# Performance work log

Measured on AMD Instinct MI355X. Metric: run time of the kernel, lower is better.

The kernel has to match this reference:

```python
import jax, jax.numpy as jnp
import numpy as np

REF_POSE = np.array([[213.33335876464844, 124.50563049316406], [190.504638671875, 115.11840057373047], [169.9791717529297, 101.77180480957031], [146.72341918945312, 96.25749206542969], [128.86770629882812, 87.2344970703125], [150.34292602539062, 101.61070251464844], [119.29926300048828, 98.73982238769531], [100.03463745117188, 99.74459838867188], [82.62400817871094, 101.2509536743164], [148.91049194335938, 112.71517181396484], [114.37303161621094, 113.20121002197266], [91.90096282958984, 116.49812316894531], [74.75020599365234, 119.37875366210938], [149.59658813476562, 124.09295654296875], [119.72419738769531, 126.36898040771484], [99.59107208251953, 129.40196228027344], [82.82524108886719, 131.584228515625], [154.55911254882812, 135.07681274414062], [133.8833770751953, 140.85983276367188], [120.45906066894531, 145.40306091308594], [106.21541595458984, 150.072265625]], dtype=np.float32)

SCALES = (0.25, 0.5, 1.0)
ORIENTATIONS = (0, 90, 180, 270)
INPUT_SIZE = (256, 256)          # (H, W)
ANCHOR_STRIDE = (1, 1)           # (y_stride, x_stride)
POS_TH = 0.5
KPT_SIGMA = 0.05                 # per-keypoint OKS falloff


def _generate_anchor_poses():
    # scale + rotate ref pose about its centroid -> [A, 21, 2]
    c = REF_POSE.mean(axis=0, keepdims=True)
    out = []
    for s in SCALES:
        for o in ORIENTATIONS:
            th = np.deg2rad(o)
            R = np.array([[np.cos(th), -np.sin(th)], [np.sin(th), np.cos(th)]], dtype=np.float32)
            out.append(c + s * (REF_POSE - c) @ R.T)
    return np.stack(out).astype(np.float32)


def _all_anchors(feat_h, feat_w):
    base = _generate_anchor_poses()                      # [A,21,2]
    w_ratio = INPUT_SIZE[1] / feat_w
    h_ratio = INPUT_SIZE[0] / feat_h
    sx = np.arange(0, feat_w, ANCHOR_STRIDE[1]) * w_ratio
    sy = np.arange(0, feat_h, ANCHOR_STRIDE[0]) * h_ratio
    gx, gy = np.meshgrid(sx, sy)
    shifts = np.stack([gx.ravel(), gy.ravel()], axis=1).astype(np.float32)  # [K,2]
    all_a = base[None, :, :, :] + shifts[:, None, None, :]                  # [K,A,21,2]
    return jnp.asarray(all_a.reshape(-1, 21, 2))                            # [K*A,21,2]


def _pose_oks(anchors, gt):
    # anchors [N,21,2], gt [B,2,21,3] -> OKS sim [B,N,2]
    d2 = jnp.sum((anchors[None, :, None, :, :] - gt[:, None, :, :, :2]) ** 2, axis=-1)  # [B,N,2,21]
    vis = (gt[..., 2] > 0).astype(anchors.dtype)[:, None, :, :]                          # [B,1,2,21]
    xy = gt[..., :2]
    area = jnp.prod(xy.max(axis=2) - xy.min(axis=2), axis=-1)                            # [B,2]
    s2 = jnp.maximum(area, 1.0)[:, None, :, None]                                        # [B,1,2,1]
    k2 = (2.0 * KPT_SIGMA) ** 2
    oks = jnp.exp(-d2 / (2.0 * s2 * k2))
    return jnp.sum(oks * vis, axis=-1) / jnp.maximum(jnp.sum(vis, axis=-1), 1.0)          # [B,N,2]


def setup_inputs() -> dict:
    key = jax.random.key(0)
    k1, k2 = jax.random.split(key)
    B = 16
    xy = jax.random.uniform(k1, (B, 42, 2), dtype=jnp.float32) * 216.0 + 20.0
    vis = jnp.ones((B, 42, 1), dtype=jnp.float32)
    pose_gt = jnp.concatenate([xy, vis], axis=-1)          # [B,42,3]
    hand_type = jnp.ones((B, 2), dtype=jnp.int32)          # both hands present
    return {"pose_gt": pose_gt, "hand_type": hand_type, "feat_h": 64, "feat_w": 64}


def reference(pose_gt, hand_type, feat_h, feat_w):
    all_anchors = _all_anchors(feat_h, feat_w)             # [N,21,2], N=K*A
    inside = jnp.sum((all_anchors[..., 0] >= 0) & (all_anchors[..., 1] >= 0)
                     & (all_anchors[..., 0] < INPUT_SIZE[0])
                     & (all_anchors[..., 1] < INPUT_SIZE[1]), axis=1) == 21  # [N]

    B = pose_gt.shape[0]
    gt = pose_gt.reshape(B, 2, 21, 3)                      # hand 0 = right, hand 1 = left
    sim = _pose_oks(all_anchors, gt)                       # [B,N,2]
    am = jnp.argmax(sim, axis=-1)                          # [B,N]
    mx = jnp.max(sim, axis=-1)                             # [B,N]

    right = (am == 0) & (mx > POS_TH) & (hand_type[:, 0:1] == 1) & inside[None, :]
    left = (am == 1) & (mx > POS_TH) & (hand_type[:, 1:2] == 1) & inside[None, :]
    neg = (~right) & (~left) & inside[None, :]

    # labels channel layout matches source: [:,:,0]=left, [:,:,1]=negative, [:,:,2]=right
    labels = jnp.stack([left, neg, right], axis=-1).astype(pose_gt.dtype)   # [B,N,3]
    labels = jnp.where(inside[None, :, None], labels, jnp.asarray(-1.0, pose_gt.dtype))

    pose_targets = (jnp.where(right[..., None, None], gt[:, 0][:, None], 0.0)
                    + jnp.where(left[..., None, None], gt[:, 1][:, None], 0.0))  # [B,N,21,3]

    offsets = pose_targets[..., :2] - all_anchors[None, :, :, :]             # [B,N,21,2]
    offsets = jnp.where(inside[None, :, None, None], offsets, 0.0)
    return all_anchors, inside, labels, offsets
```

## Files before the change

kernel.cpp:

```cpp
#include <hip/hip_runtime.h>
#include <math.h>

#define NA 49152
#define NB 16
#define ABLOCKS 192
#define EPS 1e-3f

typedef __attribute__((ext_vector_type(4))) float f4v;

__device__ __forceinline__ void nt_store4(float* p, float a, float b, float c, float d) {
  f4v v; v.x = a; v.y = b; v.z = c; v.w = d;
  __builtin_nontemporal_store(v, reinterpret_cast<f4v*>(p));
}

__constant__ float RP[21][2] = {
  {213.33335876464844f, 124.50563049316406f},
  {190.504638671875f,   115.11840057373047f},
  {169.9791717529297f,  101.77180480957031f},
  {146.72341918945312f, 96.25749206542969f},
  {128.86770629882812f, 87.2344970703125f},
  {150.34292602539062f, 101.61070251464844f},
  {119.29926300048828f, 98.73982238769531f},
  {100.03463745117188f, 99.74459838867188f},
  {82.62400817871094f,  101.2509536743164f},
  {148.91049194335938f, 112.71517181396484f},
  {114.37303161621094f, 113.20121002197266f},
  {91.90096282958984f,  116.49812316894531f},
  {74.75020599365234f,  119.37875366210938f},
  {149.59658813476562f, 124.09295654296875f},
  {119.72419738769531f, 126.36898040771484f},
  {99.59107208251953f,  129.40196228027344f},
  {82.82524108886719f,  131.584228515625f},
  {154.55911254882812f, 135.07681274414062f},
  {133.8833770751953f,  140.85983276367188f},
  {120.45906066894531f, 145.40306091308594f},
  {106.21541595458984f, 150.072265625f}
};

__device__ __forceinline__ void ref_center(float& cx, float& cy) {
  #pragma clang fp contract(off)
  float rx[8], ry[8];
  #pragma unroll
  for (int j = 0; j < 8; ++j) {
    rx[j] = RP[j][0] + RP[j + 8][0];
    ry[j] = RP[j][1] + RP[j + 8][1];
  }
  float sx = ((rx[0] + rx[1]) + (rx[2] + rx[3])) + ((rx[4] + rx[5]) + (rx[6] + rx[7]));
  float sy = ((ry[0] + ry[1]) + (ry[2] + ry[3])) + ((ry[4] + ry[5]) + (ry[6] + ry[7]));
  #pragma unroll
  for (int j = 16; j < 21; ++j) { sx += RP[j][0]; sy += RP[j][1]; }
  cx = sx / 21.0f;
  cy = sy / 21.0f;
}

__device__ __forceinline__ float2 base_pt(int p, int j, float cx, float cy) {
  #pragma clang fp contract(off)
  const int si = p >> 2, oi = p & 3;
  const float s = (si == 0) ? 0.25f : (si == 1 ? 0.5f : 1.0f);
  const float dx = s * (RP[j][0] - cx);
  const float dy = s * (RP[j][1] - cy);
  const float rx = (oi == 0) ? dx : (oi == 1 ? -dy : (oi == 2 ? -dx : dy));
  const float ry = (oi == 0) ? dy : (oi == 1 ? dx : (oi == 2 ? -dy : -dx));
  return make_float2(cx + rx, cy + ry);
}

__global__ __launch_bounds__(256, 5) void k_all(const float* __restrict__ gt,
                                                const int* __restrict__ ht,
                                                float* __restrict__ oa,
                                                float* __restrict__ oins,
                                                float* __restrict__ ol,
                                                float* __restrict__ oo) {
  __shared__ float2 sb2[252];
  __shared__ float4 sg4[21];
  __shared__ float2 sv2[21];
  __shared__ float sden[2], srden[2], snv[2];
  __shared__ int sht[2];
  __shared__ float4 sanc[256];
  __shared__ int scc[256];

  const int tid = threadIdx.x;
  const int b = blockIdx.x / ABLOCKS;
  const int ab = blockIdx.x % ABLOCKS;
  const int a0 = ab * 256;

  if (tid < 252) {
    float cx, cy; ref_center(cx, cy);
    sb2[tid] = base_pt(tid / 21, tid % 21, cx, cy);
  }
  if (tid < 21) {
    const float* g0 = gt + b * 126 + tid * 3;
    const float* g1 = g0 + 63;
    sg4[tid] = make_float4(g0[0], g0[1], g1[0], g1[1]);
    sv2[tid] = make_float2((g0[2] > 0.0f) ? 1.0f : 0.0f,
                           (g1[2] > 0.0f) ? 1.0f : 0.0f);
  }
  if (tid == 252 || tid == 253) {
    const int h = tid - 252;
    const float* g = gt + b * 126 + h * 63;
    float mnx = g[0], mxx = g[0], mny = g[1], mxy = g[1];
    float nv = (g[2] > 0.0f) ? 1.0f : 0.0f;
    for (int j = 1; j < 21; ++j) {
      float x = g[j * 3], y = g[j * 3 + 1];
      mnx = fminf(mnx, x); mxx = fmaxf(mxx, x);
      mny = fminf(mny, y); mxy = fmaxf(mxy, y);
      nv += (g[j * 3 + 2] > 0.0f) ? 1.0f : 0.0f;
    }
    const float area = (mxx - mnx) * (mxy - mny);
    const float s2 = fmaxf(area, 1.0f);
    const float den = (2.0f * s2) * 0.01f;
    sden[h] = den;
    srden[h] = -1.0f / den;
    snv[h] = fmaxf(nv, 1.0f);
  }
  if (tid == 254 || tid == 255) sht[tid - 254] = ht[b * 2 + (tid - 254)];
  __syncthreads();

  const int a = a0 + tid;
  const int p = a % 12;
  const int kc = a / 12;
  const float shx = 4.0f * (float)(kc & 63);
  const float shy = 4.0f * (float)(kc >> 6);
  const int pb = p * 21;
  sanc[tid] = make_float4(shx, shy, (float)pb, 0.0f);

  const float rd0 = srden[0], rd1 = srden[1];
  bool inside = true;
  float s0f = 0.0f, s1f = 0.0f;
  #pragma unroll
  for (int j = 0; j < 21; ++j) {
    #pragma clang fp contract(off)
    const float2 bpv = sb2[pb + j];
    const float anx = bpv.x + shx;
    const float any = bpv.y + shy;
    inside = inside && (anx >= 0.0f) && (any >= 0.0f) &&
                       (anx < 256.0f) && (any < 256.0f);
    const float4 g = sg4[j];
    const float2 v = sv2[j];
    const float dx0 = anx - g.x, dy0 = any - g.y;
    const float dx1 = anx - g.z, dy1 = any - g.w;
    s0f += __expf((dx0 * dx0 + dy0 * dy0) * rd0) * v.x;
    s1f += __expf((dx1 * dx1 + dy1 * dy1) * rd1) * v.y;
  }
  float sim0 = s0f / snv[0];
  float sim1 = s1f / snv[1];
  const float mxf = fmaxf(sim0, sim1);
  const bool need_exact = (fabsf(mxf - 0.5f) < EPS) ||
                          ((mxf > 0.5f - EPS) && (fabsf(sim0 - sim1) < EPS));

  if (__builtin_expect(need_exact, 0)) {
    #pragma clang fp contract(off)
    float q0[8], q1[8];
    #pragma unroll
    for (int j = 0; j < 16; ++j) {
      const float2 bpv = sb2[pb + j];
      const float ax = bpv.x + shx, ay = bpv.y + shy;
      const float4 g = sg4[j];
      const float2 v = sv2[j];
      float dx0 = ax - g.x, dy0 = ay - g.y;
      float d20 = dx0 * dx0 + dy0 * dy0;
      float t0 = (float)::exp((double)(-d20 / sden[0])) * v.x;
      float dx1 = ax - g.z, dy1 = ay - g.w;
      float d21 = dx1 * dx1 + dy1 * dy1;
      float t1 = (float)::exp((double)(-d21 / sden[1])) * v.y;
      if (j < 8) { q0[j] = t0; q1[j] = t1; }
      else       { q0[j - 8] += t0; q1[j - 8] += t1; }
    }
    float s0 = ((q0[0] + q0[1]) + (q0[2] + q0[3])) + ((q0[4] + q0[5]) + (q0[6] + q0[7]));
    float s1 = ((q1[0] + q1[1]) + (q1[2] + q1[3])) + ((q1[4] + q1[5]) + (q1[6] + q1[7]));
    #pragma unroll
    for (int j = 16; j < 21; ++j) {
      const float2 bpv = sb2[pb + j];
      const float ax = bpv.x + shx, ay = bpv.y + shy;
      const float4 g = sg4[j];
      const float2 v = sv2[j];
      float dx0 = ax - g.x, dy0 = ay - g.y;
      float d20 = dx0 * dx0 + dy0 * dy0;
      s0 += (float)::exp((double)(-d20 / sden[0])) * v.x;
      float dx1 = ax - g.z, dy1 = ay - g.w;
      float d21 = dx1 * dx1 + dy1 * dy1;
      s1 += (float)::exp((double)(-d21 / sden[1])) * v.y;
    }
    sim0 = s0 / snv[0];
    sim1 = s1 / snv[1];
  }

  const int am = (sim1 > sim0) ? 1 : 0;
  const float mx = fmaxf(sim0, sim1);
  const bool pos = mx > 0.5f;
  const bool right = (am == 0) && pos && (sht[0] == 1) && inside;
  const bool left  = (am == 1) && pos && (sht[1] == 1) && inside;

  int c;
  if (!inside)      c = -1;
  else if (right)   c = 1;
  else if (left)    c = 2;
  else              c = 0;
  scc[tid] = c;
  __syncthreads();

  if (tid < 192) {
    float* lb = ol + ((size_t)b * NA + a0) * 3;
    float r[4];
    #pragma unroll
    for (int k = 0; k < 4; ++k) {
      const int q = tid * 4 + k;
      const int al = q / 3;
      const int rr = q - al * 3;
      const int cc = scc[al];
      float v;
      if (cc < 0)       v = -1.0f;
      else if (rr == 0) v = (cc == 2) ? 1.0f : 0.0f;
      else if (rr == 1) v = (cc == 0) ? 1.0f : 0.0f;
      else              v = (cc == 1) ? 1.0f : 0.0f;
      r[k] = v;
    }
    nt_store4(lb + tid * 4, r[0], r[1], r[2], r[3]);
  }

  {
    float* ob = oo + ((size_t)b * NA + a0) * 42;
    int al = (2 * tid) / 21;
    int jj = 2 * tid - al * 21;
    #pragma unroll
    for (int i = 0; i < 11; ++i) {
      #pragma clang fp contract(off)
      if (i == 10 && tid >= 128) break;
      const int idx = i * 256 + tid;
      const bool w1 = (jj + 1) >= 21;
      const int al1 = al + (w1 ? 1 : 0);
      const int j1 = w1 ? 0 : (jj + 1);
      float r[4];
      {
        const float4 sa = sanc[al];
        const int cc = scc[al];
        const float2 bpv = sb2[(int)sa.z + jj];
        const float anx = bpv.x + sa.x, any = bpv.y + sa.y;
        const float4 g = sg4[jj];
        const bool has = (cc == 1) || (cc == 2);
        float tx = (cc == 2) ? g.z : g.x;
        float ty = (cc == 2) ? g.w : g.y;
        tx = has ? tx : 0.0f; ty = has ? ty : 0.0f;
        r[0] = (cc >= 0) ? (tx - anx) : 0.0f;
        r[1] = (cc >= 0) ? (ty - any) : 0.0f;
      }
      {
        const float4 sa = sanc[al1];
        const int cc = scc[al1];
        const float2 bpv = sb2[(int)sa.z + j1];
        const float anx = bpv.x + sa.x, any = bpv.y + sa.y;
        const float4 g = sg4[j1];
        const bool has = (cc == 1) || (cc == 2);
        float tx = (cc == 2) ? g.z : g.x;
        float ty = (cc == 2) ? g.w : g.y;
        tx = has ? tx : 0.0f; ty = has ? ty : 0.0f;
        r[2] = (cc >= 0) ? (tx - anx) : 0.0f;
        r[3] = (cc >= 0) ? (ty - any) : 0.0f;
      }
      nt_store4(ob + idx * 4, r[0], r[1], r[2], r[3]);
      jj += 8; al += 24;
      if (jj >= 21) { jj -= 21; ++al; }
    }
  }

  if (b == 0) {
    float* ap = oa + (size_t)a0 * 42;
    int al = (2 * tid) / 21;
    int jj = 2 * tid - al * 21;
    #pragma unroll
    for (int i = 0; i < 11; ++i) {
      if (i == 10 && tid >= 128) break;
      const int idx = i * 256 + tid;
      const bool w1 = (jj + 1) >= 21;
      const int al1 = al + (w1 ? 1 : 0);
      const int j1 = w1 ? 0 : (jj + 1);
      const float4 sa = sanc[al];
      const float2 bpv = sb2[(int)sa.z + jj];
      const float4 sb = sanc[al1];
      const float2 bq = sb2[(int)sb.z + j1];
      nt_store4(ap + idx * 4, bpv.x + sa.x, bpv.y + sa.y,
                              bq.x + sb.x,  bq.y + sb.y);
      jj += 8; al += 24;
      if (jj >= 21) { jj -= 21; ++al; }
    }
    if (tid < 64) {
      float* ib = oins + a0;
      nt_store4(ib + tid * 4,
                (scc[tid * 4]     >= 0) ? 1.0f : 0.0f,
                (scc[tid * 4 + 1] >= 0) ? 1.0f : 0.0f,
                (scc[tid * 4 + 2] >= 0) ? 1.0f : 0.0f,
                (scc[tid * 4 + 3] >= 0) ? 1.0f : 0.0f);
    }
  }
}

extern "C" void kernel_launch(void* const* d_in, const int* in_sizes, int n_in,
                              void* d_out, int out_size, void* d_ws, size_t ws_size,
                              hipStream_t stream) {
  (void)in_sizes; (void)n_in; (void)d_ws; (void)ws_size; (void)out_size;
  const float* gt = (const float*)d_in[0];
  const int* ht = (const int*)d_in[1];
  float* out = (float*)d_out;
  float* out_anchors = out;
  float* out_inside  = out + (size_t)NA * 42;
  float* out_labels  = out + (size_t)NA * 43;
  float* out_offsets = out_labels + (size_t)NB * NA * 3;

  hipLaunchKernelGGL(k_all, dim3(NB * ABLOCKS), dim3(256), 0, stream,
                     gt, ht, out_anchors, out_inside, out_labels, out_offsets);
}
```

Measured before the change: 164.5 us.

## Spread anchor/inside output writes across batch blocks and use regular stores

Anchor and inside-mask outputs were written only by the batch-0 blocks, which gave those blocks extra work. Now each of the 16 batch blocks covering an anchor range writes 1/16 of that range's anchor and inside data, which balances the per-block store load. Nontemporal stores are replaced with plain float4 stores. The per-anchor class code is packed into the w field of the sanc shared array, removing the separate scc array and its shared loads.

Result: faster. 159.9 us (-2.9%).

```diff
diff --git a/kernel.cpp b/kernel.cpp
--- a/kernel.cpp
+++ b/kernel.cpp
@@ -6,11 +6,8 @@
 #define ABLOCKS 192
 #define EPS 1e-3f
 
-typedef __attribute__((ext_vector_type(4))) float f4v;
-
-__device__ __forceinline__ void nt_store4(float* p, float a, float b, float c, float d) {
-  f4v v; v.x = a; v.y = b; v.z = c; v.w = d;
-  __builtin_nontemporal_store(v, reinterpret_cast<f4v*>(p));
+__device__ __forceinline__ void st4(float* p, float a, float b, float c, float d) {
+  *reinterpret_cast<float4*>(p) = make_float4(a, b, c, d);
 }
 
 __constant__ float RP[21][2] = {
@@ -76,7 +73,6 @@
   __shared__ float sden[2], srden[2], snv[2];
   __shared__ int sht[2];
   __shared__ float4 sanc[256];
-  __shared__ int scc[256];
 
   const int tid = threadIdx.x;
   const int b = blockIdx.x / ABLOCKS;
@@ -121,7 +117,6 @@
   const float shx = 4.0f * (float)(kc & 63);
   const float shy = 4.0f * (float)(kc >> 6);
   const int pb = p * 21;
-  sanc[tid] = make_float4(shx, shy, (float)pb, 0.0f);
 
   const float rd0 = srden[0], rd1 = srden[1];
   bool inside = true;
@@ -195,7 +190,7 @@
   else if (right)   c = 1;
   else if (left)    c = 2;
   else              c = 0;
-  scc[tid] = c;
+  sanc[tid] = make_float4(shx, shy, (float)pb, (float)c);
   __syncthreads();
 
   if (tid < 192) {
@@ -206,7 +201,7 @@
       const int q = tid * 4 + k;
       const int al = q / 3;
       const int rr = q - al * 3;
-      const int cc = scc[al];
+      const int cc = (int)sanc[al].w;
       float v;
       if (cc < 0)       v = -1.0f;
       else if (rr == 0) v = (cc == 2) ? 1.0f : 0.0f;
@@ -214,7 +209,7 @@
       else              v = (cc == 1) ? 1.0f : 0.0f;
       r[k] = v;
     }
-    nt_store4(lb + tid * 4, r[0], r[1], r[2], r[3]);
+    st4(lb + tid * 4, r[0], r[1], r[2], r[3]);
   }
 
   {
@@ -232,7 +227,7 @@
       float r[4];
       {
         const float4 sa = sanc[al];
-        const int cc = scc[al];
+        const int cc = (int)sa.w;
         const float2 bpv = sb2[(int)sa.z + jj];
         const float anx = bpv.x + sa.x, any = bpv.y + sa.y;
         const float4 g = sg4[jj];
@@ -245,7 +240,7 @@
       }
       {
         const float4 sa = sanc[al1];
-        const int cc = scc[al1];
+        const int cc = (int)sa.w;
         const float2 bpv = sb2[(int)sa.z + j1];
         const float anx = bpv.x + sa.x, any = bpv.y + sa.y;
         const float4 g = sg4[j1];
@@ -256,40 +251,35 @@
         r[2] = (cc >= 0) ? (tx - anx) : 0.0f;
         r[3] = (cc >= 0) ? (ty - any) : 0.0f;
       }
-      nt_store4(ob + idx * 4, r[0], r[1], r[2], r[3]);
+      st4(ob + idx * 4, r[0], r[1], r[2], r[3]);
       jj += 8; al += 24;
       if (jj >= 21) { jj -= 21; ++al; }
     }
   }
 
-  if (b == 0) {
+  if (tid < 168) {
     float* ap = oa + (size_t)a0 * 42;
-    int al = (2 * tid) / 21;
-    int jj = 2 * tid - al * 21;
-    #pragma unroll
-    for (int i = 0; i < 11; ++i) {
-      if (i == 10 && tid >= 128) break;
-      const int idx = i * 256 + tid;
-      const bool w1 = (jj + 1) >= 21;
-      const int al1 = al + (w1 ? 1 : 0);
-      const int j1 = w1 ? 0 : (jj + 1);
-      const float4 sa = sanc[al];
-      const float2 bpv = sb2[(int)sa.z + jj];
-      const float4 sb = sanc[al1];
-      const float2 bq = sb2[(int)sb.z + j1];
-      nt_store4(ap + idx * 4, bpv.x + sa.x, bpv.y + sa.y,
-                              bq.x + sb.x,  bq.y + sb.y);
-      jj += 8; al += 24;
-      if (jj >= 21) { jj -= 21; ++al; }
-    }
-    if (tid < 64) {
-      float* ib = oins + a0;
-      nt_store4(ib + tid * 4,
-                (scc[tid * 4]     >= 0) ? 1.0f : 0.0f,
-                (scc[tid * 4 + 1] >= 0) ? 1.0f : 0.0f,
-                (scc[tid * 4 + 2] >= 0) ? 1.0f : 0.0f,
-                (scc[tid * 4 + 3] >= 0) ? 1.0f : 0.0f);
-    }
+    const int idx = b * 168 + tid;
+    const int e0 = idx * 2;
+    const int al = e0 / 21;
+    const int jj = e0 - al * 21;
+    const bool w1 = (jj + 1) >= 21;
+    const int al1 = al + (w1 ? 1 : 0);
+    const int j1 = w1 ? 0 : (jj + 1);
+    const float4 sa = sanc[al];
+    const float2 bpv = sb2[(int)sa.z + jj];
+    const float4 sb = sanc[al1];
+    const float2 bq = sb2[(int)sb.z + j1];
+    st4(ap + idx * 4, bpv.x + sa.x, bpv.y + sa.y,
+                      bq.x + sb.x,  bq.y + sb.y);
+  }
+  if (tid < 4) {
+    const int t = b * 4 + tid;
+    st4(oins + a0 + t * 4,
+        (sanc[t * 4].w     >= 0.0f) ? 1.0f : 0.0f,
+        (sanc[t * 4 + 1].w >= 0.0f) ? 1.0f : 0.0f,
+        (sanc[t * 4 + 2].w >= 0.0f) ? 1.0f : 0.0f,
+        (sanc[t * 4 + 3].w >= 0.0f) ? 1.0f : 0.0f);
   }
 }
 
```
